# Kernel tuning notes

Hardware: AMD Instinct MI355X
Metric: run time of the kernel (lower is better)

Reference implementation:

```python
import jax, jax.numpy as jnp
import numpy as np

B, N, D, H = 2, 2048, 2048, 16
HD = D // H  # head_dim = 128


def _rope(x, cos, sin):
    # x: [B,H,N,HD]; cos/sin: [N,HD]. use_real=True, use_real_unbind_dim=-1 (interleaved pairs).
    xr = x[..., 0::2]
    xi = x[..., 1::2]
    x_rot = jnp.stack([-xi, xr], axis=-1).reshape(x.shape)
    return x * cos[None, None] + x_rot * sin[None, None]


def setup_inputs() -> dict:
    key = jax.random.key(0)
    ks = jax.random.split(key, 10)
    x = jax.random.normal(ks[0], (B, N, D), dtype=jnp.float32)
    # realistic RoPE tables
    inv_freq = 1.0 / (10000.0 ** (np.arange(0, HD, 2, dtype=np.float32) / HD))
    t = np.arange(N, dtype=np.float32)
    ang = np.einsum('n,f->nf', t, inv_freq)           # [N, HD/2]
    ang = np.repeat(ang, 2, axis=-1)                  # [N, HD] interleaved
    cos = jnp.asarray(np.cos(ang))
    sin = jnp.asarray(np.sin(ang))
    s = 0.02
    Wq = jax.random.normal(ks[1], (D, D), dtype=jnp.float32) * s
    Wk = jax.random.normal(ks[2], (D, D), dtype=jnp.float32) * s
    Wv = jax.random.normal(ks[3], (D, D), dtype=jnp.float32) * s
    Wo = jax.random.normal(ks[4], (D, D), dtype=jnp.float32) * s
    bq = jnp.zeros((D,), jnp.float32)
    bk = jnp.zeros((D,), jnp.float32)
    bv = jnp.zeros((D,), jnp.float32)
    bo = jnp.zeros((D,), jnp.float32)
    return {"x": x, "cos": cos, "sin": sin, "Wq": Wq, "bq": bq, "Wk": Wk,
            "bk": bk, "Wv": Wv, "bv": bv, "Wo": Wo, "bo": bo}


def reference(x, cos, sin, Wq, bq, Wk, bk, Wv, bv, Wo, bo):
    scale = HD ** -0.5
    q = x @ Wq + bq
    k = x @ Wk + bk
    v = x @ Wv + bv
    # b n (h c) -> b h n c
    def split_heads(t):
        return t.reshape(B, N, H, HD).transpose(0, 2, 1, 3)
    q, k, v = split_heads(q), split_heads(k), split_heads(v)
    q = q * scale  # module's dp_scale
    q = _rope(q, cos, sin)
    k = _rope(k, cos, sin)
    # flash_attn_func(softmax_scale=None) applies head_dim^-0.5 AGAIN -> effective HD^-1
    logits = jnp.einsum('bhqc,bhkc->bhqk', q, k) * scale
    attn = jax.nn.softmax(logits, axis=-1)
    o = jnp.einsum('bhqk,bhkc->bhqc', attn, v)
    o = o.transpose(0, 2, 1, 3).reshape(B, N, D)  # b h n c -> b n (h c)
    return o @ Wo + bo
```

## Files before the change

### kernel.cpp

```cpp
#include <hip/hip_runtime.h>

typedef unsigned short u16;
typedef unsigned int u32;
typedef __attribute__((ext_vector_type(8))) short bfx8;
typedef __attribute__((ext_vector_type(4))) float fx4;
typedef __attribute__((ext_vector_type(16))) float fx16;
typedef __attribute__((ext_vector_type(4))) unsigned short u16x4;

#define MFMA_BF16(a,b,c)   __builtin_amdgcn_mfma_f32_16x16x32_bf16((a),(b),(c),0,0,0)
#define MFMA32_BF16(a,b,c) __builtin_amdgcn_mfma_f32_32x32x16_bf16((a),(b),(c),0,0,0)

#define BATCH 2
#define SEQ   2048
#define DM    2048
#define NH    16
#define HD    128
#define MR    4096

__device__ __forceinline__ u16 f2bf(float f){
  union{float f; unsigned u;} v; v.f = f;
  unsigned r = v.u + 0x7FFFu + ((v.u >> 16) & 1u);
  return (u16)(r >> 16);
}
__device__ __forceinline__ unsigned cvtpk(float lo, float hi){
  unsigned r;
  asm("v_cvt_pk_bf16_f32 %0, %1, %2" : "=v"(r) : "v"(lo), "v"(hi));
  return r;
}
__device__ __forceinline__ void gll16(const void* g, void* l){
  __builtin_amdgcn_global_load_lds(
      (const __attribute__((address_space(1))) void*)g,
      (__attribute__((address_space(3))) void*)l, 16, 0, 0);
}

__global__ __launch_bounds__(256) void k_prep(const float* __restrict__ x, u16* __restrict__ xb,
                                              const float* __restrict__ Wq, const float* __restrict__ Wk,
                                              const float* __restrict__ Wv, const float* __restrict__ Wo,
                                              u16* __restrict__ Th){
  __shared__ float T[64][65];
  const int bid = blockIdx.x;
  const int t = threadIdx.x;
  if (bid < 8192){
    int gid = bid*256 + t;
    float4 v = ((const float4*)x)[gid];
    u16x4 o = {f2bf(v.x), f2bf(v.y), f2bf(v.z), f2bf(v.w)};
    ((u16x4*)xb)[gid] = o;
    return;
  }
  const int inner = (bid - 8192) & 1023;
  const int z = (bid - 8192) >> 10;
  const float* W = (z==0) ? Wq : (z==1) ? Wk : (z==2) ? Wv : Wo;
  int n0 = (inner & 31)*64, k0 = (inner >> 5)*64;
  int r = t>>2, c = (t&3)*16;
  const float* src = W + (size_t)(k0+r)*DM + n0 + c;
  #pragma unroll
  for (int j=0;j<4;j++){
    float4 v = *(const float4*)(src + 4*j);
    T[r][c+4*j+0]=v.x; T[r][c+4*j+1]=v.y; T[r][c+4*j+2]=v.z; T[r][c+4*j+3]=v.w;
  }
  __syncthreads();
  int nr = t>>2, kc = (t&3)*16;
  size_t ob = (size_t)(z*DM + n0+nr)*DM + k0 + kc;
  #pragma unroll
  for (int j=0;j<16;j+=4){
    u16x4 vh;
    #pragma unroll
    for (int q=0;q<4;q++) vh[q] = f2bf(T[kc+j+q][nr]);
    *(u16x4*)(Th+ob+j)=vh;
  }
}

__global__ __launch_bounds__(256) void k_gemm_qkv(
    const u16* __restrict__ A, const u16* __restrict__ B,
    const float* __restrict__ bqp, const float* __restrict__ bkp, const float* __restrict__ bvp,
    const float* __restrict__ cs, const float* __restrict__ sn,
    u16* __restrict__ qb, u16* __restrict__ kb, u16* __restrict__ vt)
{
  __shared__ u16 sA[128*64], sB[128*64];
  const int K = DM;
  const int tid = threadIdx.x;
  const int lane = tid & 63;
  const int w = tid >> 6;
  const int g = lane >> 4, qi = lane & 15;
  const int wr = w >> 1, wc = w & 1;
  const int bid = blockIdx.x;
  const int xcd = bid & 7, idx = bid >> 3;
  const int cx = xcd & 3, cy = xcd >> 2;
  const int bx = cx*12 + idx % 12;
  const int by = cy*16 + idx / 12;
  const int bm = by * 128;
  const int bn = bx * 128;

  int r_[4], sc_[4];
  #pragma unroll
  for (int i=0;i<4;i++){
    int off = w*4096 + i*1024 + lane*16;
    int r = off>>7, cb = off&127;
    r_[i] = r; sc_[i] = (cb ^ ((r&7)<<4)) >> 1;
  }

  fx4 acc[4][4] = {};

  for (int k0 = 0; k0 < K; k0 += 64){
    __syncthreads();
    #pragma unroll
    for (int i=0;i<4;i++){
      gll16(A + (size_t)(bm + r_[i])*K + k0 + sc_[i], &sA[w*2048 + i*512]);
      gll16(B + (size_t)(bn + r_[i])*K + k0 + sc_[i], &sB[w*2048 + i*512]);
    }
    __syncthreads();

    #pragma unroll
    for (int kk=0;kk<2;kk++){
      const int cb = kk*64 + g*16;
      bfx8 fa[4], fb[4];
      #pragma unroll
      for (int m=0;m<4;m++){
        int row = wr*64 + m*16 + qi;
        fa[m] = *(const bfx8*)((const char*)sA + row*128 + (cb ^ ((row&7)<<4)));
      }
      #pragma unroll
      for (int n=0;n<4;n++){
        int row = wc*64 + n*16 + qi;
        fb[n] = *(const bfx8*)((const char*)sB + row*128 + (cb ^ ((row&7)<<4)));
      }
      #pragma unroll
      for (int m=0;m<4;m++)
        #pragma unroll
        for (int n=0;n<4;n++)
          acc[m][n] = MFMA_BF16(fa[m], fb[n], acc[m][n]);
    }
  }

  const int sec = bn >> 11;
  if (sec < 2){
    u16* dst = sec ? kb : qb;
    const float* bias = sec ? bkp : bqp;
    const float qs = sec ? 1.0f : (1.4426950408889634f/128.0f);
    #pragma unroll
    for (int m=0;m<4;m++){
      #pragma unroll
      for (int n=0;n<4;n++){
        int col = bn + wc*64 + n*16 + qi;
        int cq = col & 2047, hh = cq>>7, d = cq&127;
        float bc = bias[cq];
        float sgn = (d&1) ? 1.0f : -1.0f;
        #pragma unroll
        for (int r=0;r<4;r++){
          int row = bm + wr*64 + m*16 + g*4 + r;
          int bI = row>>11, nr2 = row&2047;
          float v = (acc[m][n][r] + bc)*qs;
          float p = __shfl_xor(v, 1, 64);
          float c = cs[nr2*HD + d], s = sn[nr2*HD + d];
          float y = v*c + sgn*p*s;
          dst[((size_t)(bI*NH+hh)*SEQ + nr2)*HD + d] = f2bf(y);
        }
      }
    }
  } else {
    #pragma unroll
    for (int m=0;m<4;m++){
      #pragma unroll
      for (int n=0;n<4;n++){
        int col = bn + wc*64 + n*16 + qi;
        int cv = col & 2047, hh = cv>>7, d = cv&127;
        float bc = bvp[cv];
        int row0 = bm + wr*64 + m*16 + g*4;
        int bI = row0>>11, n0_ = row0&2047;
        u16x4 pk;
        #pragma unroll
        for (int r=0;r<4;r++) pk[r] = f2bf(acc[m][n][r] + bc);
        *(u16x4*)(vt + ((size_t)(bI*NH+hh)*HD + d)*SEQ + n0_) = pk;
      }
    }
  }
}

__global__ __launch_bounds__(256) void k_gemm(
    const u16* __restrict__ A, const u16* __restrict__ B,
    const float* __restrict__ bias, float* __restrict__ C,
    int M, int N, int K)
{
  __shared__ u16 sA[128*64], sB[128*64];
  const int tid = threadIdx.x;
  const int lane = tid & 63;
  const int w = tid >> 6;
  const int g = lane >> 4, qi = lane & 15;
  const int wr = w >> 1, wc = w & 1;
  const int bm = blockIdx.y * 128;
  const int bn = blockIdx.x * 128;

  int r_[4], sc_[4];
  #pragma unroll
  for (int i=0;i<4;i++){
    int off = w*4096 + i*1024 + lane*16;
    int r = off>>7, cb = off&127;
    r_[i] = r; sc_[i] = (cb ^ ((r&7)<<4)) >> 1;
  }

  fx4 acc[4][4] = {};

  for (int k0 = 0; k0 < K; k0 += 64){
    __syncthreads();
    #pragma unroll
    for (int i=0;i<4;i++){
      gll16(A + (size_t)(bm + r_[i])*K + k0 + sc_[i], &sA[w*2048 + i*512]);
      gll16(B + (size_t)(bn + r_[i])*K + k0 + sc_[i], &sB[w*2048 + i*512]);
    }
    __syncthreads();

    #pragma unroll
    for (int kk=0;kk<2;kk++){
      const int cb = kk*64 + g*16;
      bfx8 fa[4], fb[4];
      #pragma unroll
      for (int m=0;m<4;m++){
        int row = wr*64 + m*16 + qi;
        fa[m] = *(const bfx8*)((const char*)sA + row*128 + (cb ^ ((row&7)<<4)));
      }
      #pragma unroll
      for (int n=0;n<4;n++){
        int row = wc*64 + n*16 + qi;
        fb[n] = *(const bfx8*)((const char*)sB + row*128 + (cb ^ ((row&7)<<4)));
      }
      #pragma unroll
      for (int m=0;m<4;m++)
        #pragma unroll
        for (int n=0;n<4;n++)
          acc[m][n] = MFMA_BF16(fa[m], fb[n], acc[m][n]);
    }
  }

  #pragma unroll
  for (int m=0;m<4;m++){
    #pragma unroll
    for (int n=0;n<4;n++){
      int col = bn + wc*64 + n*16 + qi;
      float bc = bias[col];
      #pragma unroll
      for (int r=0;r<4;r++){
        int row = bm + wr*64 + m*16 + g*4 + r;
        C[(size_t)row*N + col] = acc[m][n][r] + bc;
      }
    }
  }
}

__global__ __launch_bounds__(128) void k_flash(const u16* __restrict__ Q, const u16* __restrict__ Kb,
                                               const u16* __restrict__ Vt, u16* __restrict__ O){
  __shared__ union SM {
    struct { u16 k[64*128]; u16 v[128*64]; } s;
    u16 ob[64*128];
  } sm;
  const int tid = threadIdx.x, lane = tid & 63, w = tid >> 6;
  const int bid0 = blockIdx.x;
  const int bid = ((bid0 & 7) << 7) | (bid0 >> 3);
  const int qt = bid & 31, h = (bid>>5)&15, b = bid>>9;
  const int bh = b*NH + h;
  const int qb0 = qt*64;
  const int hi = lane >> 5, qi = lane & 31;
  const u16* Kb2 = Kb + (size_t)bh*SEQ*HD;
  const u16* Vt2 = Vt + (size_t)bh*SEQ*HD;

  bfx8 qf[8];
  {
    const u16* qp = Q + ((size_t)bh*SEQ + qb0 + w*32 + qi)*HD + hi*8;
    #pragma unroll
    for (int ks=0; ks<8; ++ks) qf[ks] = *(const bfx8*)(qp + ks*16);
  }

  u32 koff[8], voff[8];
  #pragma unroll
  for (int i=0;i<8;i++){
    int off = w*8192 + i*1024 + lane*16;
    int kr = off>>8, kc = off&255;
    int kcs = kc ^ ((kr&15)<<4);
    koff[i] = kr*HD + (kcs>>1);
    int vr = off>>7, vc = off&127;
    int vcs = vc ^ ((vr&7)<<4);
    voff[i] = vr*SEQ + (vcs>>1);
  }

#define STAGE_K(kv_) do { _Pragma("unroll") \
    for (int i_=0;i_<8;i_++) gll16(Kb2 + koff[i_] + (u32)(kv_)*HD, &sm.s.k[w*4096 + i_*512]); } while(0)
#define STAGE_V(kv_) do { _Pragma("unroll") \
    for (int i_=0;i_<8;i_++) gll16(Vt2 + voff[i_] + (u32)(kv_),    &sm.s.v[w*4096 + i_*512]); } while(0)

  fx16 accO0 = {}, accO1 = {}, accO2 = {}, accO3 = {};
  float lrun = 0.f;

  STAGE_K(0);
  STAGE_V(0);

  for (int t=0; t<32; ++t){
    asm volatile("s_waitcnt vmcnt(8)" ::: "memory");
    __builtin_amdgcn_s_barrier();

    fx16 stA = {}, stB = {};
    __builtin_amdgcn_s_setprio(1);
    #pragma unroll
    for (int ks=0; ks<8; ++ks){
      const int cb = ks*32 + hi*16;
      int rowA = qi;
      int rowB = 32 + qi;
      bfx8 kfa = *(const bfx8*)((const char*)sm.s.k + rowA*256 + (cb ^ ((rowA&15)<<4)));
      bfx8 kfb = *(const bfx8*)((const char*)sm.s.k + rowB*256 + (cb ^ ((rowB&15)<<4)));
      stA = MFMA32_BF16(kfa, qf[ks], stA);
      stB = MFMA32_BF16(kfb, qf[ks], stB);
    }
    __builtin_amdgcn_s_setprio(0);
    __builtin_amdgcn_s_barrier();
    if (t < 31) STAGE_K(t*64 + 64);

    float ps = 0.f;
    #pragma unroll
    for (int i=0;i<16;i++){
      float p0 = exp2f(stA[i]); stA[i] = p0; ps += p0;
      float p1 = exp2f(stB[i]); stB[i] = p1; ps += p1;
    }
    lrun += ps;

    bfx8 pv0, pv1, pv2, pv3;
#define PACK(pvx_, stX_, base_) do { \
      unsigned a0 = cvtpk(stX_[base_+0], stX_[base_+1]); \
      unsigned a1 = cvtpk(stX_[base_+2], stX_[base_+3]); \
      unsigned b0 = cvtpk(stX_[base_+4], stX_[base_+5]); \
      unsigned b1 = cvtpk(stX_[base_+6], stX_[base_+7]); \
      asm volatile("v_permlane32_swap_b32 %0, %1" : "+v"(a0), "+v"(b0)); \
      asm volatile("v_permlane32_swap_b32 %0, %1" : "+v"(a1), "+v"(b1)); \
      union { bfx8 v; unsigned u[4]; } pu_; \
      pu_.u[0] = a0; pu_.u[1] = a1; pu_.u[2] = b0; pu_.u[3] = b1; \
      pvx_ = pu_.v; } while(0)
    PACK(pv0, stA, 0);
    PACK(pv1, stA, 8);
    PACK(pv2, stB, 0);
    PACK(pv3, stB, 8);
#undef PACK

    asm volatile("s_waitcnt vmcnt(8)" ::: "memory");
    if (t == 31) asm volatile("s_waitcnt vmcnt(0)" ::: "memory");
    __builtin_amdgcn_s_barrier();

    __builtin_amdgcn_s_setprio(1);
    #pragma unroll
    for (int dblk=0; dblk<4; ++dblk){
      const int row = dblk*32 + qi;
      const int swz = (row&7)<<4;
      const char* vrow = (const char*)sm.s.v + row*128;
      bfx8 vf0 = *(const bfx8*)(vrow + ((0*32 + hi*16) ^ swz));
      bfx8 vf1 = *(const bfx8*)(vrow + ((1*32 + hi*16) ^ swz));
      bfx8 vf2 = *(const bfx8*)(vrow + ((2*32 + hi*16) ^ swz));
      bfx8 vf3 = *(const bfx8*)(vrow + ((3*32 + hi*16) ^ swz));
      fx16 a = (dblk==0)?accO0:(dblk==1)?accO1:(dblk==2)?accO2:accO3;
      a = MFMA32_BF16(vf0, pv0, a);
      a = MFMA32_BF16(vf1, pv1, a);
      a = MFMA32_BF16(vf2, pv2, a);
      a = MFMA32_BF16(vf3, pv3, a);
      if (dblk==0) accO0 = a; else if (dblk==1) accO1 = a; else if (dblk==2) accO2 = a; else accO3 = a;
    }
    __builtin_amdgcn_s_setprio(0);
    __builtin_amdgcn_s_barrier();
    if (t < 31) STAGE_V(t*64 + 64);
  }
#undef STAGE_K
#undef STAGE_V

  {
    float l = lrun + __shfl_xor(lrun, 32, 64);
    float inv = 1.0f / l;
    int q = w*32 + qi;
    char* obr = (char*)sm.ob + q*256;
    const int swz = (q&7)<<4;
#define OWRITE(accX_, dblk_) do { _Pragma("unroll") \
    for (int p=0;p<8;p++){ \
      int d = dblk_*32 + 2*(p&1) + 8*(p>>1) + 4*hi; \
      unsigned wv = cvtpk(accX_[2*p]*inv, accX_[2*p+1]*inv); \
      *(unsigned*)(obr + ((d*2) ^ swz)) = wv; } } while(0)
    OWRITE(accO0, 0); OWRITE(accO1, 1); OWRITE(accO2, 2); OWRITE(accO3, 3);
#undef OWRITE
  }
  __syncthreads();
  {
    int q2 = tid>>1, c0 = (tid&1)*64;
    u16* dst = O + (size_t)(b*SEQ + qb0 + q2)*DM + h*HD + c0;
    #pragma unroll
    for (int jj=0;jj<8;jj++){
      int d0 = c0 + jj*8;
      bfx8 v = *(const bfx8*)((const char*)sm.ob + q2*256 + ((d0*2) ^ ((q2&7)<<4)));
      *(bfx8*)(dst + jj*8) = v;
    }
  }
}

extern "C" void kernel_launch(void* const* d_in, const int* in_sizes, int n_in,
                              void* d_out, int out_size, void* d_ws, size_t ws_size,
                              hipStream_t stream){
  (void)in_sizes; (void)n_in; (void)out_size; (void)ws_size;
  const float* x  = (const float*)d_in[0];
  const float* cs = (const float*)d_in[1];
  const float* sn = (const float*)d_in[2];
  const float* Wq = (const float*)d_in[3];
  const float* bq = (const float*)d_in[4];
  const float* Wk = (const float*)d_in[5];
  const float* bk = (const float*)d_in[6];
  const float* Wv = (const float*)d_in[7];
  const float* bv = (const float*)d_in[8];
  const float* Wo = (const float*)d_in[9];
  const float* bo = (const float*)d_in[10];
  float* out = (float*)d_out;

  char* ws = (char*)d_ws;
  const size_t MB = 1048576;
  u16* xb   = (u16*)(ws);
  u16* wt   = (u16*)(ws + 16*MB);
  u16* qb   = (u16*)(ws + 48*MB);
  u16* kb   = (u16*)(ws + 64*MB);
  u16* vt   = (u16*)(ws + 80*MB);
  u16* ob16 = (u16*)(ws + 96*MB);

  k_prep<<<12288,256,0,stream>>>(x, xb, Wq, Wk, Wv, Wo, wt);
  k_gemm_qkv<<<1536,256,0,stream>>>(xb, wt, bq, bk, bv, cs, sn, qb, kb, vt);

  k_flash<<<1024,128,0,stream>>>(qb, kb, vt, ob16);

  k_gemm<<<dim3(16,32),256,0,stream>>>(ob16, wt + (size_t)3*DM*DM, bo, out, MR, DM, DM);
}
```

Measured before the change: 290.8 us.

## Stage V-transpose epilogue through LDS and compute softmax row sums via MFMA

The QKV GEMM epilogue for the V slice now writes the tile into a swizzled shared-memory buffer and then emits coalesced 16-byte stores along the sequence dimension, replacing scattered 8-byte transposed stores. In attention, the per-lane softmax denominator sum is replaced by an extra MFMA against a vector of ones, so the row sums come out of the matrix unit, which removes the VALU adds and the cross-lane shuffle. This adds four MFMAs per KV tile and sums the bf16-rounded probabilities, which slightly changes numerics but matches the values actually multiplied into V.

```diff
diff --git a/kernel.cpp b/kernel.cpp
--- a/kernel.cpp
+++ b/kernel.cpp
@@ -76,7 +76,9 @@
     const float* __restrict__ cs, const float* __restrict__ sn,
     u16* __restrict__ qb, u16* __restrict__ kb, u16* __restrict__ vt)
 {
-  __shared__ u16 sA[128*64], sB[128*64];
+  __shared__ u16 smem[2*128*64];
+  u16* sA = smem;
+  u16* sB = smem + 128*64;
   const int K = DM;
   const int tid = threadIdx.x;
   const int lane = tid & 63;
@@ -158,20 +160,31 @@
       }
     }
   } else {
+    __syncthreads();
     #pragma unroll
     for (int m=0;m<4;m++){
       #pragma unroll
       for (int n=0;n<4;n++){
-        int col = bn + wc*64 + n*16 + qi;
-        int cv = col & 2047, hh = cv>>7, d = cv&127;
-        float bc = bvp[cv];
-        int row0 = bm + wr*64 + m*16 + g*4;
-        int bI = row0>>11, n0_ = row0&2047;
+        int dl = wc*64 + n*16 + qi;
+        float bc = bvp[(bn & 2047) + dl];
+        int row0 = wr*64 + m*16 + g*4;
         u16x4 pk;
         #pragma unroll
         for (int r=0;r<4;r++) pk[r] = f2bf(acc[m][n][r] + bc);
-        *(u16x4*)(vt + ((size_t)(bI*NH+hh)*HD + d)*SEQ + n0_) = pk;
-      }
+        *(u16x4*)((char*)smem + dl*256 + ((row0*2) ^ ((dl&7)<<4))) = pk;
+      }
+    }
+    __syncthreads();
+    const int hh = (bn & 2047) >> 7;
+    const int bI = bm >> 11;
+    const int nbase = bm & 2047;
+    u16* vb = vt + (size_t)(bI*NH + hh)*HD*SEQ + nbase;
+    #pragma unroll
+    for (int jj=0;jj<8;jj++){
+      int dg = jj*16 + (tid>>4);
+      int ch = tid & 15;
+      bfx8 v = *(const bfx8*)((const char*)smem + dg*256 + ((ch*16) ^ ((dg&7)<<4)));
+      *(bfx8*)(vb + (size_t)dg*SEQ + ch*8) = v;
     }
   }
 }
@@ -269,6 +282,10 @@
     for (int ks=0; ks<8; ++ks) qf[ks] = *(const bfx8*)(qp + ks*16);
   }
 
+  union { unsigned u[4]; bfx8 v; } on_;
+  on_.u[0] = on_.u[1] = on_.u[2] = on_.u[3] = 0x3F803F80u;
+  const bfx8 vone = on_.v;
+
   u32 koff[8], voff[8];
   #pragma unroll
   for (int i=0;i<8;i++){
@@ -287,7 +304,7 @@
     for (int i_=0;i_<8;i_++) gll16(Vt2 + voff[i_] + (u32)(kv_),    &sm.s.v[w*4096 + i_*512]); } while(0)
 
   fx16 accO0 = {}, accO1 = {}, accO2 = {}, accO3 = {};
-  float lrun = 0.f;
+  fx16 accL = {};
 
   STAGE_K(0);
   STAGE_V(0);
@@ -312,13 +329,11 @@
     __builtin_amdgcn_s_barrier();
     if (t < 31) STAGE_K(t*64 + 64);
 
-    float ps = 0.f;
     #pragma unroll
     for (int i=0;i<16;i++){
-      float p0 = exp2f(stA[i]); stA[i] = p0; ps += p0;
-      float p1 = exp2f(stB[i]); stB[i] = p1; ps += p1;
-    }
-    lrun += ps;
+      stA[i] = exp2f(stA[i]);
+      stB[i] = exp2f(stB[i]);
+    }
 
     bfx8 pv0, pv1, pv2, pv3;
 #define PACK(pvx_, stX_, base_) do { \
@@ -358,6 +373,10 @@
       a = MFMA32_BF16(vf3, pv3, a);
       if (dblk==0) accO0 = a; else if (dblk==1) accO1 = a; else if (dblk==2) accO2 = a; else accO3 = a;
     }
+    accL = MFMA32_BF16(vone, pv0, accL);
+    accL = MFMA32_BF16(vone, pv1, accL);
+    accL = MFMA32_BF16(vone, pv2, accL);
+    accL = MFMA32_BF16(vone, pv3, accL);
     __builtin_amdgcn_s_setprio(0);
     __builtin_amdgcn_s_barrier();
     if (t < 31) STAGE_V(t*64 + 64);
@@ -366,8 +385,7 @@
 #undef STAGE_V
 
   {
-    float l = lrun + __shfl_xor(lrun, 32, 64);
-    float inv = 1.0f / l;
+    float inv = 1.0f / accL[0];
     int q = w*32 + qi;
     char* obr = (char*)sm.ob + q*256;
     const int swz = (q&7)<<4;
```

Result: slower. 313.9 us (+7.9%).
